# Kernel tuning notes

Measured on AMD Instinct MI355X. Metric: run time of the kernel, lower is better.

The kernel has to match this reference:

```python
import jax, jax.numpy as jnp
import numpy as np

N, K, E, H, I = 8192, 2, 8, 2048, 1408


def setup_inputs() -> dict:
    key = jax.random.key(0)
    k1, k2, k3, k4, k5 = jax.random.split(key, 5)
    x = jax.random.normal(k1, (N, H), dtype=jnp.float32)
    topk_indices = jax.random.randint(k2, (N, K), 0, E, dtype=jnp.int32)
    topk_weights = jax.random.uniform(k3, (N, K), dtype=jnp.float32)
    # normalize routing weights per token (typical top-k softmax output scale)
    topk_weights = topk_weights / jnp.sum(topk_weights, axis=-1, keepdims=True)
    scale = 0.02  # typical init std, keeps activations well-scaled
    gate_up_proj = jax.random.normal(k4, (E, H, 2 * I), dtype=jnp.float32) * scale
    down_proj = jax.random.normal(k5, (E, I, H), dtype=jnp.float32) * scale
    return {"x": x, "topk_indices": topk_indices, "topk_weights": topk_weights,
            "gate_up_proj": gate_up_proj, "down_proj": down_proj}


def reference(x, topk_indices, topk_weights, gate_up_proj, down_proj):
    """MoE experts: route -> grouped GEMM SwiGLU -> grouped GEMM -> weighted unroute.

    x: [N, H]; topk_indices/topk_weights: [N, K];
    gate_up_proj: [E, H, 2I]; down_proj: [E, I, H].
    """
    n, k = topk_indices.shape
    e = gate_up_proj.shape[0]
    flat_e = topk_indices.reshape(-1)                 # [N*K] expert id per routed slot
    sort_idx = jnp.argsort(flat_e)                    # stable sort: group slots by expert
    token_idx = sort_idx // k                         # source token for each sorted slot
    sorted_tokens = x[token_idx]                      # [N*K, H]
    group_sizes = jnp.bincount(flat_e, length=e).astype(jnp.int32)  # [E]
    # grouped (ragged) GEMM over contiguous expert groups
    h = jax.lax.ragged_dot(sorted_tokens, gate_up_proj, group_sizes)  # [N*K, 2I]
    gate_h, up_h = jnp.split(h, 2, axis=-1)
    intermediate = jax.nn.silu(gate_h) * up_h          # fused SwiGLU
    out_sorted = jax.lax.ragged_dot(intermediate, down_proj, group_sizes)  # [N*K, H]
    # weighted scatter-combine back to token order
    w_sorted = topk_weights.reshape(-1)[sort_idx]      # [N*K]
    out = jnp.zeros_like(x).at[token_idx].add(out_sorted * w_sorted[:, None])
    return out
```

## Files before the change

kernel.cpp:

```cpp
#include <hip/hip_runtime.h>


#define N_TOK 8192
#define TOPK  2
#define NEXP  8
#define HD    2048
#define ID    1408
#define NK    (N_TOK * TOPK)
#define MAXRT 136

typedef __bf16 bf16x8 __attribute__((ext_vector_type(8)));
typedef float  f32x4  __attribute__((ext_vector_type(4)));

__device__ __forceinline__ float b2f(unsigned short u) {
    union { unsigned int i; float f; } v; v.i = ((unsigned int)u) << 16; return v.f;
}
__device__ __forceinline__ unsigned short f2b(float f) {
    union { float f; unsigned int i; } v; v.f = f;
    unsigned int x = v.i;
    return (unsigned short)((x + 0x7fffu + ((x >> 16) & 1u)) >> 16);
}

__device__ __forceinline__ void glds16(const void* g, void* l) {
    __builtin_amdgcn_global_load_lds(
        (const __attribute__((address_space(1))) unsigned int*)g,
        (__attribute__((address_space(3))) unsigned int*)l,
        16, 0, 0);
}


__global__ void probe_k(const unsigned short* __restrict__ xu, int* __restrict__ mode) {
    __shared__ int c;
    if (threadIdx.x == 0) c = 0;
    __syncthreads();
    float a = fabsf(b2f(xu[threadIdx.x * 2]));
    int sane = (a > 1e-4f && a < 100.f) ? 1 : 0;
    atomicAdd(&c, sane);
    __syncthreads();
    if (threadIdx.x == 0) mode[0] = (c < 512) ? 1 : 0;
}


__global__ void convert_x(const void* __restrict__ x, unsigned short* __restrict__ xb,
                          const int* __restrict__ mode) {
    int gid = blockIdx.x * 256 + threadIdx.x;
    size_t o = (size_t)gid * 8;
    if (mode[0]) {
        const float* f = (const float*)x + o;
        float4 f0 = *(const float4*)f;
        float4 f1 = *(const float4*)(f + 4);
        uint4 v;
        v.x = f2b(f0.x) | ((unsigned int)f2b(f0.y) << 16);
        v.y = f2b(f0.z) | ((unsigned int)f2b(f0.w) << 16);
        v.z = f2b(f1.x) | ((unsigned int)f2b(f1.y) << 16);
        v.w = f2b(f1.z) | ((unsigned int)f2b(f1.w) << 16);
        *(uint4*)(xb + o) = v;
    } else {
        *(uint4*)(xb + o) = *(const uint4*)((const unsigned short*)x + o);
    }
}


__global__ void init_k(int* cnt, int* fill) {
    int t = threadIdx.x;
    if (t < NEXP) { cnt[t] = 0; fill[t] = 0; }
}

__global__ void route_count(const int* __restrict__ idx, int* __restrict__ cnt) {
    int s = blockIdx.x * 256 + threadIdx.x;
    if (s < NK) atomicAdd(&cnt[idx[s]], 1);
}

__global__ void route_scan(const int* __restrict__ cnt, int* __restrict__ base,
                           int* __restrict__ tb) {
    if (threadIdx.x == 0) {
        int acc = 0, tacc = 0;
        for (int e = 0; e < NEXP; e++) {
            base[e] = acc; tb[e] = tacc;
            acc += cnt[e]; tacc += (cnt[e] + 127) >> 7;
        }
        base[NEXP] = acc; tb[NEXP] = tacc;
    }
}

__global__ void route_scatter(const int* __restrict__ idx,
                              const int* __restrict__ base,
                              int* __restrict__ fill,
                              int* __restrict__ tok,
                              int* __restrict__ inv) {
    int s = blockIdx.x * 256 + threadIdx.x;
    if (s < NK) {
        int e = idx[s];
        int p = base[e] + atomicAdd(&fill[e], 1);
        tok[p] = s >> 1;
        inv[s] = p;
    }
}


__global__ void transpose_k(const void* __restrict__ in, unsigned short* __restrict__ out,
                            int R, int C, const int* __restrict__ mode) {
    __shared__ float tile[64][65];
    bool fp32m = (mode[0] != 0);
    int e  = blockIdx.z;
    int c0 = blockIdx.x * 64, r0 = blockIdx.y * 64;
    int t = threadIdx.x;
    if (fp32m) {
        const float* inp = (const float*)in + (size_t)e * R * C;
        for (int i = 0; i < 16; i++) {
            int lin = t + i * 256;
            int r = lin >> 6, c = lin & 63;
            tile[r][c] = inp[(size_t)(r0 + r) * C + c0 + c];
        }
    } else {
        const unsigned int* inp = (const unsigned int*)in + (size_t)e * R * (C >> 1);
        for (int i = 0; i < 8; i++) {
            int lin = t + i * 256;
            int r = lin >> 5, cu = lin & 31;
            unsigned int v = inp[(size_t)(r0 + r) * (C >> 1) + (c0 >> 1) + cu];
            tile[r][2 * cu]     = b2f((unsigned short)(v & 0xffffu));
            tile[r][2 * cu + 1] = b2f((unsigned short)(v >> 16));
        }
    }
    __syncthreads();
    unsigned int* outp = (unsigned int*)out + (size_t)e * C * (R >> 1);
    for (int i = 0; i < 8; i++) {
        int lin = t + i * 256;
        int c = lin >> 5, ru = lin & 31;
        unsigned int lo = f2b(tile[2 * ru][c]);
        unsigned int hi = f2b(tile[2 * ru + 1][c]);
        outp[(size_t)(c0 + c) * (R >> 1) + (r0 >> 1) + ru] = lo | (hi << 16);
    }
}



template<int KD, int ND, int LDA, bool GATHER>
__launch_bounds__(256, 2)
__global__ void gemm_k(const unsigned short* __restrict__ A,
                       const unsigned short* __restrict__ B,
                       const int* __restrict__ base,
                       const int* __restrict__ tb,
                       const int* __restrict__ tok,
                       unsigned short* __restrict__ C) {
    const int CT = ND / 128;
    int G = gridDim.x;
    int orig = blockIdx.x;
    int q8 = G >> 3, r8 = G & 7, xcd = orig & 7, lin = orig >> 3;
    int wgid = (xcd < r8 ? xcd * (q8 + 1) : r8 * (q8 + 1) + (xcd - r8) * q8) + lin;
    int ct  = wgid % CT;
    int rtf = wgid / CT;
    if (rtf >= tb[NEXP]) return;
    int e = 0;
    while (tb[e + 1] <= rtf) e++;
    int row0 = base[e] + (rtf - tb[e]) * 128;
    int rend = base[e + 1];

    __shared__ unsigned short As[2][128 * 64];
    __shared__ unsigned short Bs[2][128 * 64];

    int tid  = threadIdx.x;
    int lane = tid & 63;
    int wave = tid >> 6;
    int wm = wave & 1, wn = wave >> 1;
    int l15 = lane & 15, qq = lane >> 4;

    const unsigned short* bptr = B + (size_t)e * ND * KD + (size_t)(ct * 128) * KD;

    const unsigned short* agp[4];
    int boff[4];
    int wslot[4];
    for (int i = 0; i < 4; i++) {
        int s = i * 256 + wave * 64 + lane;
        int r = s >> 3;
        int c = (s & 7) ^ (r & 7);
        int p = row0 + r;
        bool sv = (p < rend);
        const unsigned short* arow;
        if (GATHER) arow = sv ? A + (size_t)tok[p] * LDA : A;
        else        arow = sv ? A + (size_t)p * LDA      : A;
        agp[i]  = arow + c * 8;
        boff[i] = r * KD + c * 8;
        wslot[i] = (i * 256 + wave * 64) * 8;
    }

    int arow_[4], brow_[4];
    for (int mt = 0; mt < 4; mt++) arow_[mt] = wm * 64 + mt * 16 + l15;
    for (int nt = 0; nt < 4; nt++) brow_[nt] = wn * 64 + nt * 16 + l15;

    f32x4 acc[4][4];
    for (int mt = 0; mt < 4; mt++)
        for (int nt = 0; nt < 4; nt++) acc[mt][nt] = (f32x4){0.f, 0.f, 0.f, 0.f};

#define STAGE(buf, kk)                                          \
    for (int i = 0; i < 4; i++) {                               \
        glds16(agp[i] + (kk),            &As[buf][wslot[i]]);   \
        glds16(bptr + boff[i] + (kk),    &Bs[buf][wslot[i]]);   \
    }

    STAGE(0, 0);
    __builtin_amdgcn_sched_barrier(0);
    asm volatile("s_waitcnt vmcnt(0)" ::: "memory");
    __builtin_amdgcn_s_barrier();
    __builtin_amdgcn_sched_barrier(0);

    int cur = 0;
    for (int k0 = 0; k0 < KD; k0 += 64) {
        if (k0 + 64 < KD) { STAGE(cur ^ 1, k0 + 64); }
        for (int ks = 0; ks < 2; ks++) {
            int kc = ks * 4 + qq;
            bf16x8 af[4], bq[4];
            for (int mt = 0; mt < 4; mt++)
                af[mt] = *(bf16x8*)&As[cur][(arow_[mt] * 8 + (kc ^ (arow_[mt] & 7))) * 8];
            for (int nt = 0; nt < 4; nt++)
                bq[nt] = *(bf16x8*)&Bs[cur][(brow_[nt] * 8 + (kc ^ (brow_[nt] & 7))) * 8];
            for (int mt = 0; mt < 4; mt++)
                for (int nt = 0; nt < 4; nt++)
                    acc[mt][nt] = __builtin_amdgcn_mfma_f32_16x16x32_bf16(
                        af[mt], bq[nt], acc[mt][nt], 0, 0, 0);
        }
        __builtin_amdgcn_sched_barrier(0);
        asm volatile("s_waitcnt vmcnt(0)" ::: "memory");
        __builtin_amdgcn_s_barrier();
        __builtin_amdgcn_sched_barrier(0);
        cur ^= 1;
    }
#undef STAGE

    for (int mt = 0; mt < 4; mt++) {
        int rb = wm * 64 + mt * 16 + qq * 4;
        for (int reg = 0; reg < 4; reg++) {
            int p = row0 + rb + reg;
            if (p >= rend) continue;
            for (int nt = 0; nt < 4; nt++) {
                int col = ct * 128 + wn * 64 + nt * 16 + l15;
                C[(size_t)p * ND + col] = f2b(acc[mt][nt][reg]);
            }
        }
    }
}


__global__ void swiglu_k(unsigned short* __restrict__ h) {
    int gid = blockIdx.x * 256 + threadIdx.x;
    int row = gid >> 8;
    row = gid / (ID / 8);
    int c8 = (gid - row * (ID / 8)) * 8;
    unsigned short* hr = h + (size_t)row * (2 * ID);
    uint4 gv = *(const uint4*)(hr + c8);
    uint4 uv = *(const uint4*)(hr + ID + c8);
    const unsigned short* ga = (const unsigned short*)&gv;
    const unsigned short* ua = (const unsigned short*)&uv;
    uint4 o;
    unsigned int* ro = (unsigned int*)&o;
    for (int i = 0; i < 4; i++) {
        float g0 = b2f(ga[2 * i]),     u0 = b2f(ua[2 * i]);
        float g1 = b2f(ga[2 * i + 1]), u1 = b2f(ua[2 * i + 1]);
        float s0 = (g0 / (1.f + __expf(-g0))) * u0;
        float s1 = (g1 / (1.f + __expf(-g1))) * u1;
        ro[i] = f2b(s0) | ((unsigned int)f2b(s1) << 16);
    }
    *(uint4*)(hr + c8) = o;
}


__global__ void combine_k(const unsigned short* __restrict__ outs,
                          const int* __restrict__ inv,
                          const void* __restrict__ w,
                          void* __restrict__ out,
                          const int* __restrict__ mode) {
    bool fp32m = (mode[0] != 0);
    int gid = blockIdx.x * 256 + threadIdx.x;
    int t  = gid >> 8;
    int c8 = (gid & 255) * 8;
    int p0 = inv[t * 2], p1 = inv[t * 2 + 1];
    float w0, w1;
    if (fp32m) {
        const float* wf = (const float*)w;
        w0 = wf[t * 2]; w1 = wf[t * 2 + 1];
    } else {
        const unsigned short* wu = (const unsigned short*)w;
        w0 = b2f(wu[t * 2]); w1 = b2f(wu[t * 2 + 1]);
    }
    uint4 v0 = *(const uint4*)(outs + (size_t)p0 * HD + c8);
    uint4 v1 = *(const uint4*)(outs + (size_t)p1 * HD + c8);
    const unsigned short* a = (const unsigned short*)&v0;
    const unsigned short* b = (const unsigned short*)&v1;
    float r[8];
    for (int i = 0; i < 8; i++) r[i] = w0 * b2f(a[i]) + w1 * b2f(b[i]);
    if (fp32m) {
        float* of = (float*)out + (size_t)t * HD + c8;
        *(float4*)of       = make_float4(r[0], r[1], r[2], r[3]);
        *(float4*)(of + 4) = make_float4(r[4], r[5], r[6], r[7]);
    } else {
        uint4 o;
        unsigned int* ro = (unsigned int*)&o;
        for (int i = 0; i < 4; i++)
            ro[i] = f2b(r[2 * i]) | ((unsigned int)f2b(r[2 * i + 1]) << 16);
        *(uint4*)((unsigned short*)out + (size_t)t * HD + c8) = o;
    }
}


extern "C" void kernel_launch(void* const* d_in, const int* in_sizes, int n_in,
                              void* d_out, int out_size, void* d_ws, size_t ws_size,
                              hipStream_t stream) {
    const void* x   = d_in[0];
    const int*  idx = (const int*)d_in[1];
    const void* w   = d_in[2];
    const void* gup = d_in[3];
    const void* dwn = d_in[4];

    char* ws = (char*)d_ws;
    int* mode = (int*)(ws);
    int* cnt  = (int*)(ws + 64);
    int* base = (int*)(ws + 128);
    int* fill = (int*)(ws + 192);
    int* tb   = (int*)(ws + 256);
    int* tok  = (int*)(ws + 512);
    int* inv  = (int*)(ws + 512 + 4 * NK);
    unsigned short* h    = (unsigned short*)(ws + 262144);
    unsigned short* xb   = h    + (size_t)NK * 2 * ID;
    unsigned short* dwnT = xb   + (size_t)N_TOK * HD;
    unsigned short* gupT = dwnT + (size_t)NEXP * HD * ID;
    unsigned short* outs = gupT;

    probe_k<<<1, 1024, 0, stream>>>((const unsigned short*)x, mode);
    convert_x<<<(N_TOK * HD / 8) / 256, 256, 0, stream>>>(x, xb, mode);

    init_k<<<1, 64, 0, stream>>>(cnt, fill);
    route_count<<<NK / 256, 256, 0, stream>>>(idx, cnt);
    route_scan<<<1, 64, 0, stream>>>(cnt, base, tb);
    route_scatter<<<NK / 256, 256, 0, stream>>>(idx, base, fill, tok, inv);

    transpose_k<<<dim3(2 * ID / 64, HD / 64, NEXP), 256, 0, stream>>>(
        gup, gupT, HD, 2 * ID, mode);
    transpose_k<<<dim3(HD / 64, ID / 64, NEXP), 256, 0, stream>>>(
        dwn, dwnT, ID, HD, mode);

    gemm_k<HD, 2 * ID, HD, true><<<MAXRT * (2 * ID / 128), 256, 0, stream>>>(
        xb, gupT, base, tb, tok, h);
    swiglu_k<<<(NK * (ID / 8)) / 256, 256, 0, stream>>>(h);
    gemm_k<ID, HD, 2 * ID, false><<<MAXRT * (HD / 128), 256, 0, stream>>>(
        h, dwnT, base, tb, tok, outs);

    combine_k<<<(N_TOK * HD / 8) / 256, 256, 0, stream>>>(outs, inv, w, d_out, mode);
}
```

Baseline: 989.3 us.

## Use 256x256 tiles with 8-wave ping-pong pipelined grouped GEMM

Replaces the 128x128, 4-wave grouped GEMM with a 256x256-tile, 8-wave kernel. It uses 128 KB of dynamic LDS, staged half-tile loads interleaved with MFMA phases, partial vmcnt waits and setprio around MFMA bursts. Routing tile counts are now rounded to 256 rows. The goal is higher arithmetic intensity per loaded byte and better overlap of global-to-LDS loads with compute. The cost is more padding waste for ragged expert groups, fewer workgroups, and heavier register and LDS use that limits occupancy.

```diff
diff --git a/kernel.cpp b/kernel.cpp
--- a/kernel.cpp
+++ b/kernel.cpp
@@ -7,7 +7,7 @@
 #define HD    2048
 #define ID    1408
 #define NK    (N_TOK * TOPK)
-#define MAXRT 136
+#define NT256 (NK / 256 + NEXP)
 
 typedef __bf16 bf16x8 __attribute__((ext_vector_type(8)));
 typedef float  f32x4  __attribute__((ext_vector_type(4)));
@@ -77,7 +77,7 @@
         int acc = 0, tacc = 0;
         for (int e = 0; e < NEXP; e++) {
             base[e] = acc; tb[e] = tacc;
-            acc += cnt[e]; tacc += (cnt[e] + 127) >> 7;
+            acc += cnt[e]; tacc += (cnt[e] + 255) >> 8;
         }
         base[NEXP] = acc; tb[NEXP] = tacc;
     }
@@ -136,14 +136,16 @@
 
 
 template<int KD, int ND, int LDA, bool GATHER>
-__launch_bounds__(256, 2)
-__global__ void gemm_k(const unsigned short* __restrict__ A,
-                       const unsigned short* __restrict__ B,
-                       const int* __restrict__ base,
-                       const int* __restrict__ tb,
-                       const int* __restrict__ tok,
-                       unsigned short* __restrict__ C) {
-    const int CT = ND / 128;
+__launch_bounds__(512, 2)
+__global__ void gemm8_k(const unsigned short* __restrict__ A,
+                        const unsigned short* __restrict__ B,
+                        const int* __restrict__ base,
+                        const int* __restrict__ tb,
+                        const int* __restrict__ tok,
+                        unsigned short* __restrict__ C) {
+    extern __shared__ unsigned short lds[];
+    const int CT = ND / 256;
+    const int KT = KD / 64;
     int G = gridDim.x;
     int orig = blockIdx.x;
     int q8 = G >> 3, r8 = G & 7, xcd = orig & 7, lin = orig >> 3;
@@ -153,88 +155,135 @@
     if (rtf >= tb[NEXP]) return;
     int e = 0;
     while (tb[e + 1] <= rtf) e++;
-    int row0 = base[e] + (rtf - tb[e]) * 128;
+    int row0 = base[e] + (rtf - tb[e]) * 256;
     int rend = base[e + 1];
-
-    __shared__ unsigned short As[2][128 * 64];
-    __shared__ unsigned short Bs[2][128 * 64];
 
     int tid  = threadIdx.x;
     int lane = tid & 63;
     int wave = tid >> 6;
-    int wm = wave & 1, wn = wave >> 1;
+    int wm16 = (wave & 1) * 16;
+    int wn16 = (wave >> 1) * 16;
     int l15 = lane & 15, qq = lane >> 4;
-
-    const unsigned short* bptr = B + (size_t)e * ND * KD + (size_t)(ct * 128) * KD;
-
-    const unsigned short* agp[4];
-    int boff[4];
-    int wslot[4];
-    for (int i = 0; i < 4; i++) {
-        int s = i * 256 + wave * 64 + lane;
+    int l7  = l15 & 7;
+
+    const unsigned short* bbase = B + (size_t)e * ND * KD + (size_t)(ct * 256) * KD;
+
+    const unsigned short* agp[2][2];
+    const unsigned short* bgp[2][2];
+    for (int j = 0; j < 2; j++) {
+        int s = j * 512 + tid;
         int r = s >> 3;
         int c = (s & 7) ^ (r & 7);
-        int p = row0 + r;
-        bool sv = (p < rend);
-        const unsigned short* arow;
-        if (GATHER) arow = sv ? A + (size_t)tok[p] * LDA : A;
-        else        arow = sv ? A + (size_t)p * LDA      : A;
-        agp[i]  = arow + c * 8;
-        boff[i] = r * KD + c * 8;
-        wslot[i] = (i * 256 + wave * 64) * 8;
-    }
-
-    int arow_[4], brow_[4];
-    for (int mt = 0; mt < 4; mt++) arow_[mt] = wm * 64 + mt * 16 + l15;
-    for (int nt = 0; nt < 4; nt++) brow_[nt] = wn * 64 + nt * 16 + l15;
-
-    f32x4 acc[4][4];
-    for (int mt = 0; mt < 4; mt++)
-        for (int nt = 0; nt < 4; nt++) acc[mt][nt] = (f32x4){0.f, 0.f, 0.f, 0.f};
-
-#define STAGE(buf, kk)                                          \
-    for (int i = 0; i < 4; i++) {                               \
-        glds16(agp[i] + (kk),            &As[buf][wslot[i]]);   \
-        glds16(bptr + boff[i] + (kk),    &Bs[buf][wslot[i]]);   \
-    }
-
-    STAGE(0, 0);
+        for (int h = 0; h < 2; h++) {
+            int p = row0 + h * 128 + r;
+            bool sv = (p < rend);
+            const unsigned short* ar;
+            if (GATHER) ar = sv ? A + (size_t)tok[p] * LDA : A;
+            else        ar = sv ? A + (size_t)p * LDA      : A;
+            agp[j][h] = ar + c * 8;
+            bgp[j][h] = bbase + (size_t)(h * 128 + r) * KD + c * 8;
+        }
+    }
+    int wbase = wave * 512;
+
+    f32x4 acc[8][4];
+#pragma unroll
+    for (int m = 0; m < 8; m++)
+#pragma unroll
+        for (int n = 0; n < 4; n++) acc[m][n] = (f32x4){0.f, 0.f, 0.f, 0.f};
+
+    bf16x8 af0[2], af1[2], bq[4][2];
+
+#define STAGE_A(buf, h, kt) do { int _k = ((kt) < KT ? (kt) : KT - 1) * 64;     \
+    glds16(agp[0][h] + _k, &lds[(buf) * 16384 + (h) * 8192 + wbase]);           \
+    glds16(agp[1][h] + _k, &lds[(buf) * 16384 + (h) * 8192 + 4096 + wbase]); } while (0)
+#define STAGE_B(buf, h, kt) do { int _k = ((kt) < KT ? (kt) : KT - 1) * 64;     \
+    glds16(bgp[0][h] + _k, &lds[32768 + (buf) * 16384 + (h) * 8192 + wbase]);   \
+    glds16(bgp[1][h] + _k, &lds[32768 + (buf) * 16384 + (h) * 8192 + 4096 + wbase]); } while (0)
+
+#define ALDS(buf, m, ks) (*(const bf16x8*)&lds[(buf) * 16384 +                  \
+    (((m) * 32 + wm16 + l15) * 8 + ((((ks) * 4) + qq) ^ l7)) * 8])
+#define BLDS(buf, n, ks) (*(const bf16x8*)&lds[32768 + (buf) * 16384 +          \
+    (((n) * 64 + wn16 + l15) * 8 + ((((ks) * 4) + qq) ^ l7)) * 8])
+
+#define PH_READA(buf, m0)                                                       \
+    af0[0] = ALDS(buf, m0, 0); af0[1] = ALDS(buf, m0, 1);                       \
+    af1[0] = ALDS(buf, (m0) + 1, 0); af1[1] = ALDS(buf, (m0) + 1, 1);
+#define PH_READB(buf)                                                           \
+    _Pragma("unroll") for (int n = 0; n < 4; n++) {                             \
+        bq[n][0] = BLDS(buf, n, 0); bq[n][1] = BLDS(buf, n, 1); }
+
+#define MFMA16(m0) do {                                                         \
+    _Pragma("unroll") for (int n = 0; n < 4; n++) {                             \
+        acc[m0][n] = __builtin_amdgcn_mfma_f32_16x16x32_bf16(af0[0], bq[n][0], acc[m0][n], 0, 0, 0);         \
+        acc[m0][n] = __builtin_amdgcn_mfma_f32_16x16x32_bf16(af0[1], bq[n][1], acc[m0][n], 0, 0, 0);         \
+        acc[(m0) + 1][n] = __builtin_amdgcn_mfma_f32_16x16x32_bf16(af1[0], bq[n][0], acc[(m0) + 1][n], 0, 0, 0); \
+        acc[(m0) + 1][n] = __builtin_amdgcn_mfma_f32_16x16x32_bf16(af1[1], bq[n][1], acc[(m0) + 1][n], 0, 0, 0); } } while (0)
+
+#define SYNCA(m0)                                                               \
+    __builtin_amdgcn_sched_barrier(0);                                          \
+    __builtin_amdgcn_s_barrier();                                               \
+    asm volatile("s_waitcnt lgkmcnt(0)" ::: "memory");                          \
+    __builtin_amdgcn_sched_barrier(0);                                          \
+    __builtin_amdgcn_s_setprio(1);                                              \
+    MFMA16(m0);                                                                 \
+    __builtin_amdgcn_s_setprio(0);                                              \
+    __builtin_amdgcn_sched_barrier(0);                                          \
+    __builtin_amdgcn_s_barrier();
+
+#define SYNCV(m0)                                                               \
+    __builtin_amdgcn_sched_barrier(0);                                          \
+    asm volatile("s_waitcnt vmcnt(6)" ::: "memory");                            \
+    __builtin_amdgcn_s_barrier();                                               \
+    asm volatile("s_waitcnt lgkmcnt(0)" ::: "memory");                          \
+    __builtin_amdgcn_sched_barrier(0);                                          \
+    __builtin_amdgcn_s_setprio(1);                                              \
+    MFMA16(m0);                                                                 \
+    __builtin_amdgcn_s_setprio(0);                                              \
+    __builtin_amdgcn_sched_barrier(0);                                          \
+    __builtin_amdgcn_s_barrier();
+
+    STAGE_A(0, 0, 0); STAGE_A(0, 1, 0); STAGE_B(0, 0, 0); STAGE_B(0, 1, 0);
+    STAGE_B(1, 0, 1); STAGE_B(1, 1, 1); STAGE_A(1, 0, 1);
     __builtin_amdgcn_sched_barrier(0);
-    asm volatile("s_waitcnt vmcnt(0)" ::: "memory");
+    asm volatile("s_waitcnt vmcnt(6)" ::: "memory");
     __builtin_amdgcn_s_barrier();
     __builtin_amdgcn_sched_barrier(0);
 
-    int cur = 0;
-    for (int k0 = 0; k0 < KD; k0 += 64) {
-        if (k0 + 64 < KD) { STAGE(cur ^ 1, k0 + 64); }
-        for (int ks = 0; ks < 2; ks++) {
-            int kc = ks * 4 + qq;
-            bf16x8 af[4], bq[4];
-            for (int mt = 0; mt < 4; mt++)
-                af[mt] = *(bf16x8*)&As[cur][(arow_[mt] * 8 + (kc ^ (arow_[mt] & 7))) * 8];
-            for (int nt = 0; nt < 4; nt++)
-                bq[nt] = *(bf16x8*)&Bs[cur][(brow_[nt] * 8 + (kc ^ (brow_[nt] & 7))) * 8];
-            for (int mt = 0; mt < 4; mt++)
-                for (int nt = 0; nt < 4; nt++)
-                    acc[mt][nt] = __builtin_amdgcn_mfma_f32_16x16x32_bf16(
-                        af[mt], bq[nt], acc[mt][nt], 0, 0, 0);
-        }
-        __builtin_amdgcn_sched_barrier(0);
-        asm volatile("s_waitcnt vmcnt(0)" ::: "memory");
-        __builtin_amdgcn_s_barrier();
-        __builtin_amdgcn_sched_barrier(0);
-        cur ^= 1;
-    }
-#undef STAGE
-
-    for (int mt = 0; mt < 4; mt++) {
-        int rb = wm * 64 + mt * 16 + qq * 4;
+    for (int i = 0; i < KT / 2; i++) {
+        int t1 = 2 * i + 1, t2 = 2 * i + 2, t3 = 2 * i + 3;
+        PH_READB(0); PH_READA(0, 0); STAGE_A(1, 1, t1); SYNCA(0);
+        PH_READA(0, 2);              STAGE_B(0, 0, t2); SYNCA(2);
+        PH_READA(0, 4);              STAGE_B(0, 1, t2); SYNCA(4);
+        PH_READA(0, 6);              STAGE_A(0, 0, t2); SYNCV(6);
+        PH_READB(1); PH_READA(1, 0); STAGE_A(0, 1, t2); SYNCA(0);
+        PH_READA(1, 2);              STAGE_B(1, 0, t3); SYNCA(2);
+        PH_READA(1, 4);              STAGE_B(1, 1, t3); SYNCA(4);
+        PH_READA(1, 6);              STAGE_A(1, 0, t3); SYNCV(6);
+    }
+    asm volatile("s_waitcnt vmcnt(0)" ::: "memory");
+
+#undef STAGE_A
+#undef STAGE_B
+#undef ALDS
+#undef BLDS
+#undef PH_READA
+#undef PH_READB
+#undef MFMA16
+#undef SYNCA
+#undef SYNCV
+
+#pragma unroll
+    for (int m = 0; m < 8; m++) {
+        int rbase = row0 + m * 32 + wm16 + qq * 4;
+#pragma unroll
         for (int reg = 0; reg < 4; reg++) {
-            int p = row0 + rb + reg;
+            int p = rbase + reg;
             if (p >= rend) continue;
-            for (int nt = 0; nt < 4; nt++) {
-                int col = ct * 128 + wn * 64 + nt * 16 + l15;
-                C[(size_t)p * ND + col] = f2b(acc[mt][nt][reg]);
+#pragma unroll
+            for (int n = 0; n < 4; n++) {
+                int col = ct * 256 + n * 64 + wn16 + l15;
+                C[(size_t)p * ND + col] = f2b(acc[m][n][reg]);
             }
         }
     }
@@ -243,8 +292,7 @@
 
 __global__ void swiglu_k(unsigned short* __restrict__ h) {
     int gid = blockIdx.x * 256 + threadIdx.x;
-    int row = gid >> 8;
-    row = gid / (ID / 8);
+    int row = gid / (ID / 8);
     int c8 = (gid - row * (ID / 8)) * 8;
     unsigned short* hr = h + (size_t)row * (2 * ID);
     uint4 gv = *(const uint4*)(hr + c8);
@@ -325,6 +373,17 @@
     unsigned short* gupT = dwnT + (size_t)NEXP * HD * ID;
     unsigned short* outs = gupT;
 
+    static bool attr_done = false;
+    if (!attr_done) {
+        hipFuncSetAttribute(
+            reinterpret_cast<const void*>(&gemm8_k<HD, 2 * ID, HD, true>),
+            hipFuncAttributeMaxDynamicSharedMemorySize, 131072);
+        hipFuncSetAttribute(
+            reinterpret_cast<const void*>(&gemm8_k<ID, HD, 2 * ID, false>),
+            hipFuncAttributeMaxDynamicSharedMemorySize, 131072);
+        attr_done = true;
+    }
+
     probe_k<<<1, 1024, 0, stream>>>((const unsigned short*)x, mode);
     convert_x<<<(N_TOK * HD / 8) / 256, 256, 0, stream>>>(x, xb, mode);
 
@@ -338,11 +397,11 @@
     transpose_k<<<dim3(HD / 64, ID / 64, NEXP), 256, 0, stream>>>(
         dwn, dwnT, ID, HD, mode);
 
-    gemm_k<HD, 2 * ID, HD, true><<<MAXRT * (2 * ID / 128), 256, 0, stream>>>(
-        xb, gupT, base, tb, tok, h);
+    gemm8_k<HD, 2 * ID, HD, true>
+        <<<NT256 * (2 * ID / 256), 512, 131072, stream>>>(xb, gupT, base, tb, tok, h);
     swiglu_k<<<(NK * (ID / 8)) / 256, 256, 0, stream>>>(h);
-    gemm_k<ID, HD, 2 * ID, false><<<MAXRT * (HD / 128), 256, 0, stream>>>(
-        h, dwnT, base, tb, tok, outs);
+    gemm8_k<ID, HD, 2 * ID, false>
+        <<<NT256 * (HD / 256), 512, 131072, stream>>>(h, dwnT, base, tb, tok, outs);
 
     combine_k<<<(N_TOK * HD / 8) / 256, 256, 0, stream>>>(outs, inv, w, d_out, mode);
 }
```

Result: faster. 941.3 us (-4.9%).
